# Optimization experiments

Hardware: AMD Instinct MI355X
Metric: run time of the kernel (lower is better)

## Reference

```python
import jax, jax.numpy as jnp
import numpy as np

B = 8192
I = 1024  # input_size
H = 1024  # hidden_size


def setup_inputs() -> dict:
    key = jax.random.key(0)
    ks = jax.random.split(key, 8)
    s_i = 1.0 / np.sqrt(I)
    s_h = 1.0 / np.sqrt(H)
    return {
        "x": jax.random.normal(ks[0], (B, I), dtype=jnp.float32),
        "h": jax.random.normal(ks[1], (B, H), dtype=jnp.float32),
        # nn.Linear weights have shape [out, in]; y = x @ W.T
        "W_wz": jax.random.uniform(ks[2], (H, I), jnp.float32, -s_i, s_i),
        "W_uz": jax.random.uniform(ks[3], (H, H), jnp.float32, -s_h, s_h),
        "W_wr": jax.random.uniform(ks[4], (H, I), jnp.float32, -s_i, s_i),
        "W_ur": jax.random.uniform(ks[5], (H, H), jnp.float32, -s_h, s_h),
        "W_u": jax.random.uniform(ks[6], (H, H), jnp.float32, -s_h, s_h),
        "W_w": jax.random.uniform(ks[7], (H, I), jnp.float32, -s_i, s_i),
    }


def reference(x, h, W_wz, W_uz, W_wr, W_ur, W_u, W_w):
    # Fuse the three x-projections and the two h-projections into grouped GEMMs.
    # [B, 3H] = x @ [I, 3H]
    xp = x @ jnp.concatenate([W_wz, W_wr, W_w], axis=0).T
    hp = h @ jnp.concatenate([W_uz, W_ur], axis=0).T  # [B, 2H]
    z = jax.nn.sigmoid(xp[:, :H] + hp[:, :H])
    r = jax.nn.sigmoid(xp[:, H:2 * H] + hp[:, H:])
    h_t = jnp.tanh((r * h) @ W_u.T + xp[:, 2 * H:])
    return z * h + (1.0 - z) * h_t
```

## Files before the change

kernel.cpp:

```cpp
#include <hip/hip_runtime.h>

typedef unsigned short u16;
typedef __attribute__((ext_vector_type(8))) short bf16x8;
typedef __attribute__((ext_vector_type(4))) float f32x4;

__device__ __forceinline__ u16 f2b(float f) {
  unsigned u = __float_as_uint(f);
  u += 0x7FFFu + ((u >> 16) & 1u);
  return (u16)(u >> 16);
}
__device__ __forceinline__ float sigm(float x) { return 1.0f / (1.0f + __expf(-x)); }
__device__ __forceinline__ float tanh_f(float x) { return 1.0f - 2.0f / (__expf(2.0f * x) + 1.0f); }

__device__ __forceinline__ void cp16(const u16* g, u16* l) {
  __builtin_amdgcn_global_load_lds(
      (const __attribute__((address_space(1))) unsigned int*)g,
      (__attribute__((address_space(3))) unsigned int*)l, 16, 0, 0);
}

__device__ __forceinline__ int swz(int b) {
  return b ^ (((b >> 7) & 3) << 5) ^ (((b >> 9) & 1) << 4);
}

__global__ __launch_bounds__(256) void pack_xh(const float* __restrict__ x,
                                               const float* __restrict__ h,
                                               u16* __restrict__ xhb) {
  int idx = blockIdx.x * 256 + threadIdx.x;
  int row = idx >> 9;
  int k = (idx & 511) << 2;
  const float* src = (k < 1024) ? (x + row * 1024 + k) : (h + row * 1024 + (k - 1024));
  float4 v = *reinterpret_cast<const float4*>(src);
  ushort4 o = make_ushort4(f2b(v.x), f2b(v.y), f2b(v.z), f2b(v.w));
  *reinterpret_cast<ushort4*>(xhb + ((size_t)idx << 2)) = o;
}

__global__ __launch_bounds__(256) void pack_w1(const float* __restrict__ Wwz,
                                               const float* __restrict__ Wuz,
                                               const float* __restrict__ Wwr,
                                               const float* __restrict__ Wur,
                                               const float* __restrict__ Ww,
                                               u16* __restrict__ W1b) {
  int idx = blockIdx.x * 256 + threadIdx.x;
  int n = idx >> 9;
  int k = (idx & 511) << 2;
  float4 v = make_float4(0.f, 0.f, 0.f, 0.f);
  if (n < 1024) {
    v = (k < 1024) ? *reinterpret_cast<const float4*>(Wwz + n * 1024 + k)
                   : *reinterpret_cast<const float4*>(Wuz + n * 1024 + (k - 1024));
  } else if (n < 2048) {
    int nn = n - 1024;
    v = (k < 1024) ? *reinterpret_cast<const float4*>(Wwr + nn * 1024 + k)
                   : *reinterpret_cast<const float4*>(Wur + nn * 1024 + (k - 1024));
  } else {
    int nn = n - 2048;
    if (k < 1024) v = *reinterpret_cast<const float4*>(Ww + nn * 1024 + k);
  }
  ushort4 o = make_ushort4(f2b(v.x), f2b(v.y), f2b(v.z), f2b(v.w));
  *reinterpret_cast<ushort4*>(W1b + ((size_t)idx << 2)) = o;
}

__global__ __launch_bounds__(256) void pack_wu(const float* __restrict__ Wu,
                                               u16* __restrict__ Wub) {
  int idx = blockIdx.x * 256 + threadIdx.x;
  float4 v = *reinterpret_cast<const float4*>(Wu + ((size_t)idx << 2));
  ushort4 o = make_ushort4(f2b(v.x), f2b(v.y), f2b(v.z), f2b(v.w));
  *reinterpret_cast<ushort4*>(Wub + ((size_t)idx << 2)) = o;
}

__device__ __forceinline__ void body(int t, int NT,
                                     const u16* __restrict__ Ag, const u16* __restrict__ Bg,
                                     int lda, int ldb,
                                     const u16* Ar, const u16* Br, u16* Aw, u16* Bw,
                                     int r0, int c2, int arl0, int arl1,
                                     int wr, int wc, int tid, f32x4 acc[4][4]) {
  const int ab = wr * 4096;
  const int bb = wc * 4096;
  bf16x8 af0[2][2], bfr[4][2];
#pragma unroll
  for (int mm = 0; mm < 2; ++mm) {
    af0[mm][0] = *reinterpret_cast<const bf16x8*>(Ar + ab + mm * 1024 + arl0);
    af0[mm][1] = *reinterpret_cast<const bf16x8*>(Ar + ab + mm * 1024 + arl1);
  }
#pragma unroll
  for (int nf = 0; nf < 4; ++nf) {
    bfr[nf][0] = *reinterpret_cast<const bf16x8*>(Br + bb + nf * 1024 + arl0);
    bfr[nf][1] = *reinterpret_cast<const bf16x8*>(Br + bb + nf * 1024 + arl1);
  }
  if (t + 1 < NT) {
    const u16* g0 = Ag + (size_t)r0 * lda + c2 + (size_t)(t + 1) * 64;
    u16* l0 = Aw + tid * 8;
    cp16(g0, l0); cp16(g0 + (size_t)64 * lda, l0 + 4096);
    const u16* g1 = Ag + (size_t)(128 + r0) * lda + c2 + (size_t)(t + 1) * 64;
    u16* l1 = Aw + 8192 + tid * 8;
    cp16(g1, l1); cp16(g1 + (size_t)64 * lda, l1 + 4096);
  }
  __builtin_amdgcn_s_barrier();
  __builtin_amdgcn_s_setprio(1);
#pragma unroll
  for (int mm = 0; mm < 2; ++mm)
#pragma unroll
    for (int nf = 0; nf < 4; ++nf)
#pragma unroll
      for (int ks = 0; ks < 2; ++ks)
        acc[mm][nf] = __builtin_amdgcn_mfma_f32_16x16x32_bf16(
            af0[mm][ks], bfr[nf][ks], acc[mm][nf], 0, 0, 0);
  __builtin_amdgcn_s_setprio(0);
  __builtin_amdgcn_s_barrier();
  bf16x8 af1[2][2];
#pragma unroll
  for (int mm = 0; mm < 2; ++mm) {
    af1[mm][0] = *reinterpret_cast<const bf16x8*>(Ar + ab + (2 + mm) * 1024 + arl0);
    af1[mm][1] = *reinterpret_cast<const bf16x8*>(Ar + ab + (2 + mm) * 1024 + arl1);
  }
  if (t + 2 < NT) {
    const u16* g = Bg + (size_t)r0 * ldb + c2 + (size_t)(t + 2) * 64;
    u16* l = Bw + tid * 8;
    cp16(g, l); cp16(g + (size_t)64 * ldb, l + 4096);
    asm volatile("s_waitcnt vmcnt(2)" ::: "memory");
  } else {
    asm volatile("s_waitcnt vmcnt(0)" ::: "memory");
  }
  __builtin_amdgcn_s_barrier();
  __builtin_amdgcn_s_setprio(1);
#pragma unroll
  for (int mm = 0; mm < 2; ++mm)
#pragma unroll
    for (int nf = 0; nf < 4; ++nf)
#pragma unroll
      for (int ks = 0; ks < 2; ++ks)
        acc[2 + mm][nf] = __builtin_amdgcn_mfma_f32_16x16x32_bf16(
            af1[mm][ks], bfr[nf][ks], acc[2 + mm][nf], 0, 0, 0);
  __builtin_amdgcn_s_setprio(0);
  __builtin_amdgcn_s_barrier();
}

__device__ __forceinline__ void core(const u16* __restrict__ Ag, const u16* __restrict__ Bg,
                                     int lda, int ldb, int NT,
                                     u16* As0, u16* As1, u16* Bs0, u16* Bs1,
                                     f32x4 acc[4][4]) {
  const int tid = threadIdx.x;
  const int lane = tid & 63;
  const int wid = tid >> 6;
  const int wr = wid >> 1;
  const int wc = wid & 1;

  const int plo = tid * 16;
  const int olo = swz(plo);
  const int r0 = olo >> 7;
  const int c2 = (olo & 127) >> 1;

  const int frow = lane & 15;
  const int fcb = (lane >> 4) * 16;
  const int mask = ((frow & 3) << 5) | (((frow >> 2) & 1) << 4);
  const int arl0 = (frow * 128 + ((fcb + 0) ^ mask)) >> 1;
  const int arl1 = (frow * 128 + ((fcb + 64) ^ mask)) >> 1;

  {
    const u16* g; u16* l;
    g = Ag + (size_t)r0 * lda + c2;          l = As0 + tid * 8;        cp16(g, l); cp16(g + (size_t)64 * lda, l + 4096);
    g = Ag + (size_t)(128 + r0) * lda + c2;  l = As0 + 8192 + tid * 8; cp16(g, l); cp16(g + (size_t)64 * lda, l + 4096);
    g = Bg + (size_t)r0 * ldb + c2;          l = Bs0 + tid * 8;        cp16(g, l); cp16(g + (size_t)64 * ldb, l + 4096);
    g = Bg + (size_t)r0 * ldb + c2 + 64;     l = Bs1 + tid * 8;        cp16(g, l); cp16(g + (size_t)64 * ldb, l + 4096);
  }
  asm volatile("s_waitcnt vmcnt(2)" ::: "memory");
  __builtin_amdgcn_s_barrier();

  for (int u = 0; u < NT; u += 2) {
    body(u,     NT, Ag, Bg, lda, ldb, As0, Bs0, As1, Bs0, r0, c2, arl0, arl1, wr, wc, tid, acc);
    body(u + 1, NT, Ag, Bg, lda, ldb, As1, Bs1, As0, Bs1, r0, c2, arl0, arl1, wr, wc, tid, acc);
  }
}

#define CORE_PRE()                                           \
  __shared__ u16 As0[16384];                                 \
  __shared__ u16 As1[16384];                                 \
  __shared__ u16 Bs0[8192];                                  \
  __shared__ u16 Bs1[8192];                                  \
  f32x4 acc[4][4];                                           \
  _Pragma("unroll") for (int m = 0; m < 4; ++m)              \
  _Pragma("unroll") for (int n = 0; n < 4; ++n)              \
      acc[m][n] = (f32x4){0.f, 0.f, 0.f, 0.f};

__global__ __launch_bounds__(512, 2) void gemm_zr(const u16* __restrict__ xhb,
                                                  const u16* __restrict__ W1b,
                                                  const float* __restrict__ h,
                                                  float* __restrict__ zout,
                                                  u16* __restrict__ rhb) {
  int b = blockIdx.x;
  int wg = (b & 7) * 64 + (b >> 3);
  int nb = wg >> 5, mb = wg & 31;
  const int m0 = mb * 256, n0 = nb * 128;
  CORE_PRE();
  core(xhb + (size_t)m0 * 2048, W1b + (size_t)n0 * 2048, 2048, 2048, 32,
       As0, As1, Bs0, Bs1, acc);

  const int lane = threadIdx.x & 63;
  const int wid = threadIdx.x >> 6;
  const int wr = wid >> 1, wc = wid & 1;
  const int rbase = m0 + wr * 64 + ((lane >> 4) << 2);
  const int cbase = n0 + wc * 64 + (lane & 15);
  const int isz = (n0 < 1024);
#pragma unroll
  for (int m = 0; m < 4; ++m) {
#pragma unroll
    for (int nf = 0; nf < 4; ++nf) {
      const int col = cbase + nf * 16;
#pragma unroll
      for (int j = 0; j < 4; ++j) {
        const int row = rbase + m * 16 + j;
        const float v = acc[m][nf][j];
        if (isz) {
          zout[(size_t)row * 1024 + col] = sigm(v);
        } else {
          const size_t idx = (size_t)row * 1024 + (col - 1024);
          rhb[idx] = f2b(sigm(v) * h[idx]);
        }
      }
    }
  }
}

__global__ __launch_bounds__(512, 2) void gemm_w(const u16* __restrict__ xhb,
                                                 const u16* __restrict__ W1b,
                                                 float* __restrict__ xwb) {
  int b = blockIdx.x;
  int wg = (b & 7) * 32 + (b >> 3);
  int nb = wg >> 5, mb = wg & 31;
  const int m0 = mb * 256, n0 = nb * 128;
  CORE_PRE();
  core(xhb + (size_t)m0 * 2048, W1b + (size_t)(2048 + n0) * 2048, 2048, 2048, 16,
       As0, As1, Bs0, Bs1, acc);

  const int lane = threadIdx.x & 63;
  const int wid = threadIdx.x >> 6;
  const int wr = wid >> 1, wc = wid & 1;
  const int rbase = m0 + wr * 64 + ((lane >> 4) << 2);
  const int cbase = n0 + wc * 64 + (lane & 15);
#pragma unroll
  for (int m = 0; m < 4; ++m)
#pragma unroll
    for (int nf = 0; nf < 4; ++nf)
#pragma unroll
      for (int j = 0; j < 4; ++j)
        xwb[(size_t)(rbase + m * 16 + j) * 1024 + cbase + nf * 16] = acc[m][nf][j];
}

__global__ __launch_bounds__(512, 2) void gemm2_k(const u16* __restrict__ rhb,
                                                  const u16* __restrict__ Wub,
                                                  const float* __restrict__ h,
                                                  const float* __restrict__ xwb,
                                                  float* __restrict__ out) {
  int b = blockIdx.x;
  int wg = (b & 7) * 32 + (b >> 3);
  int nb = wg >> 5, mb = wg & 31;
  const int m0 = mb * 256, n0 = nb * 128;
  CORE_PRE();
  core(rhb + (size_t)m0 * 1024, Wub + (size_t)n0 * 1024, 1024, 1024, 16,
       As0, As1, Bs0, Bs1, acc);

  const int lane = threadIdx.x & 63;
  const int wid = threadIdx.x >> 6;
  const int wr = wid >> 1, wc = wid & 1;
  const int rbase = m0 + wr * 64 + ((lane >> 4) << 2);
  const int cbase = n0 + wc * 64 + (lane & 15);
#pragma unroll
  for (int m = 0; m < 4; ++m) {
#pragma unroll
    for (int nf = 0; nf < 4; ++nf) {
      const int col = cbase + nf * 16;
#pragma unroll
      for (int j = 0; j < 4; ++j) {
        const int row = rbase + m * 16 + j;
        const size_t idx = (size_t)row * 1024 + col;
        const float z = out[idx];
        const float hv = h[idx];
        const float ht = tanh_f(acc[m][nf][j] + xwb[idx]);
        out[idx] = z * hv + (1.0f - z) * ht;
      }
    }
  }
}

extern "C" void kernel_launch(void* const* d_in, const int* in_sizes, int n_in,
                              void* d_out, int out_size, void* d_ws, size_t ws_size,
                              hipStream_t stream) {
  const float* x   = (const float*)d_in[0];
  const float* h   = (const float*)d_in[1];
  const float* Wwz = (const float*)d_in[2];
  const float* Wuz = (const float*)d_in[3];
  const float* Wwr = (const float*)d_in[4];
  const float* Wur = (const float*)d_in[5];
  const float* Wu  = (const float*)d_in[6];
  const float* Ww  = (const float*)d_in[7];
  float* out = (float*)d_out;

  char* ws = (char*)d_ws;
  u16*   xhb = (u16*)(ws);
  u16*   W1b = (u16*)(ws + 33554432);
  u16*   Wub = (u16*)(ws + 46137344);
  u16*   rhb = (u16*)(ws + 48234496);
  float* xwb = (float*)(ws + 65011712);

  pack_xh<<<16384, 256, 0, stream>>>(x, h, xhb);
  pack_w1<<<6144, 256, 0, stream>>>(Wwz, Wuz, Wwr, Wur, Ww, W1b);
  pack_wu<<<1024, 256, 0, stream>>>(Wu, Wub);
  gemm_zr<<<512, 512, 0, stream>>>(xhb, W1b, h, out, rhb);
  gemm_w<<<256, 512, 0, stream>>>(xhb, W1b, xwb);
  gemm2_k<<<256, 512, 0, stream>>>(rhb, Wub, h, xwb, out);
}
```

Baseline: 336.0 us.

## Triple-buffer GEMM LDS pipeline, remap block tiles, store x-projection in bf16

The GEMM main loop moves from double to triple buffering in LDS, so A and B tiles are prefetched two k-steps ahead, with a relaxed vmcnt wait placed after the MFMAs. The block-index to tile mapping is swapped so consecutive workgroups walk the N dimension instead of M, which changes L2 reuse. The intermediate x@W_w projection is stored as bf16 instead of fp32 to halve its write and read traffic. LDS use per block rises to about 144KB, which likely stops two 512-thread blocks from fitting on one CU, and the bf16 intermediate adds rounding error.

```diff
diff --git a/kernel.cpp b/kernel.cpp
--- a/kernel.cpp
+++ b/kernel.cpp
@@ -9,6 +9,7 @@
   u += 0x7FFFu + ((u >> 16) & 1u);
   return (u16)(u >> 16);
 }
+__device__ __forceinline__ float b2f(u16 v) { return __uint_as_float(((unsigned)v) << 16); }
 __device__ __forceinline__ float sigm(float x) { return 1.0f / (1.0f + __expf(-x)); }
 __device__ __forceinline__ float tanh_f(float x) { return 1.0f - 2.0f / (__expf(2.0f * x) + 1.0f); }
 
@@ -75,6 +76,7 @@
                                      int wr, int wc, int tid, f32x4 acc[4][4]) {
   const int ab = wr * 4096;
   const int bb = wc * 4096;
+  const bool pf = (t + 2 < NT);
   bf16x8 af0[2][2], bfr[4][2];
 #pragma unroll
   for (int mm = 0; mm < 2; ++mm) {
@@ -86,11 +88,11 @@
     bfr[nf][0] = *reinterpret_cast<const bf16x8*>(Br + bb + nf * 1024 + arl0);
     bfr[nf][1] = *reinterpret_cast<const bf16x8*>(Br + bb + nf * 1024 + arl1);
   }
-  if (t + 1 < NT) {
-    const u16* g0 = Ag + (size_t)r0 * lda + c2 + (size_t)(t + 1) * 64;
+  if (pf) {
+    const u16* g0 = Ag + (size_t)r0 * lda + c2 + (size_t)(t + 2) * 64;
     u16* l0 = Aw + tid * 8;
     cp16(g0, l0); cp16(g0 + (size_t)64 * lda, l0 + 4096);
-    const u16* g1 = Ag + (size_t)(128 + r0) * lda + c2 + (size_t)(t + 1) * 64;
+    const u16* g1 = Ag + (size_t)(128 + r0) * lda + c2 + (size_t)(t + 2) * 64;
     u16* l1 = Aw + 8192 + tid * 8;
     cp16(g1, l1); cp16(g1 + (size_t)64 * lda, l1 + 4096);
   }
@@ -112,13 +114,10 @@
     af1[mm][0] = *reinterpret_cast<const bf16x8*>(Ar + ab + (2 + mm) * 1024 + arl0);
     af1[mm][1] = *reinterpret_cast<const bf16x8*>(Ar + ab + (2 + mm) * 1024 + arl1);
   }
-  if (t + 2 < NT) {
+  if (pf) {
     const u16* g = Bg + (size_t)r0 * ldb + c2 + (size_t)(t + 2) * 64;
     u16* l = Bw + tid * 8;
     cp16(g, l); cp16(g + (size_t)64 * ldb, l + 4096);
-    asm volatile("s_waitcnt vmcnt(2)" ::: "memory");
-  } else {
-    asm volatile("s_waitcnt vmcnt(0)" ::: "memory");
   }
   __builtin_amdgcn_s_barrier();
   __builtin_amdgcn_s_setprio(1);
@@ -131,12 +130,15 @@
         acc[2 + mm][nf] = __builtin_amdgcn_mfma_f32_16x16x32_bf16(
             af1[mm][ks], bfr[nf][ks], acc[2 + mm][nf], 0, 0, 0);
   __builtin_amdgcn_s_setprio(0);
+  if (pf) asm volatile("s_waitcnt vmcnt(6)" ::: "memory");
+  else    asm volatile("s_waitcnt vmcnt(0)" ::: "memory");
   __builtin_amdgcn_s_barrier();
 }
 
 __device__ __forceinline__ void core(const u16* __restrict__ Ag, const u16* __restrict__ Bg,
                                      int lda, int ldb, int NT,
-                                     u16* As0, u16* As1, u16* Bs0, u16* Bs1,
+                                     u16* As0, u16* As1, u16* As2,
+                                     u16* Bs0, u16* Bs1, u16* Bs2,
                                      f32x4 acc[4][4]) {
   const int tid = threadIdx.x;
   const int lane = tid & 63;
@@ -155,27 +157,41 @@
   const int arl0 = (frow * 128 + ((fcb + 0) ^ mask)) >> 1;
   const int arl1 = (frow * 128 + ((fcb + 64) ^ mask)) >> 1;
 
-  {
-    const u16* g; u16* l;
-    g = Ag + (size_t)r0 * lda + c2;          l = As0 + tid * 8;        cp16(g, l); cp16(g + (size_t)64 * lda, l + 4096);
-    g = Ag + (size_t)(128 + r0) * lda + c2;  l = As0 + 8192 + tid * 8; cp16(g, l); cp16(g + (size_t)64 * lda, l + 4096);
-    g = Bg + (size_t)r0 * ldb + c2;          l = Bs0 + tid * 8;        cp16(g, l); cp16(g + (size_t)64 * ldb, l + 4096);
-    g = Bg + (size_t)r0 * ldb + c2 + 64;     l = Bs1 + tid * 8;        cp16(g, l); cp16(g + (size_t)64 * ldb, l + 4096);
-  }
-  asm volatile("s_waitcnt vmcnt(2)" ::: "memory");
-  __builtin_amdgcn_s_barrier();
-
-  for (int u = 0; u < NT; u += 2) {
-    body(u,     NT, Ag, Bg, lda, ldb, As0, Bs0, As1, Bs0, r0, c2, arl0, arl1, wr, wc, tid, acc);
-    body(u + 1, NT, Ag, Bg, lda, ldb, As1, Bs1, As0, Bs1, r0, c2, arl0, arl1, wr, wc, tid, acc);
+  auto stA = [&](u16* buf, int tg) {
+    const u16* g0 = Ag + (size_t)r0 * lda + c2 + (size_t)tg * 64;
+    u16* l0 = buf + tid * 8;
+    cp16(g0, l0); cp16(g0 + (size_t)64 * lda, l0 + 4096);
+    const u16* g1 = Ag + (size_t)(128 + r0) * lda + c2 + (size_t)tg * 64;
+    u16* l1 = buf + 8192 + tid * 8;
+    cp16(g1, l1); cp16(g1 + (size_t)64 * lda, l1 + 4096);
+  };
+  auto stB = [&](u16* buf, int tg) {
+    const u16* g = Bg + (size_t)r0 * ldb + c2 + (size_t)tg * 64;
+    u16* l = buf + tid * 8;
+    cp16(g, l); cp16(g + (size_t)64 * ldb, l + 4096);
+  };
+
+  stA(As0, 0); stB(Bs0, 0);
+  stA(As1, 1); stB(Bs1, 1);
+  asm volatile("s_waitcnt vmcnt(6)" ::: "memory");
+  __builtin_amdgcn_s_barrier();
+
+  for (int u = 0; u < NT; u += 3) {
+    body(u, NT, Ag, Bg, lda, ldb, As0, Bs0, As2, Bs2, r0, c2, arl0, arl1, wr, wc, tid, acc);
+    if (u + 1 < NT)
+      body(u + 1, NT, Ag, Bg, lda, ldb, As1, Bs1, As0, Bs0, r0, c2, arl0, arl1, wr, wc, tid, acc);
+    if (u + 2 < NT)
+      body(u + 2, NT, Ag, Bg, lda, ldb, As2, Bs2, As1, Bs1, r0, c2, arl0, arl1, wr, wc, tid, acc);
   }
 }
 
 #define CORE_PRE()                                           \
   __shared__ u16 As0[16384];                                 \
   __shared__ u16 As1[16384];                                 \
+  __shared__ u16 As2[16384];                                 \
   __shared__ u16 Bs0[8192];                                  \
   __shared__ u16 Bs1[8192];                                  \
+  __shared__ u16 Bs2[8192];                                  \
   f32x4 acc[4][4];                                           \
   _Pragma("unroll") for (int m = 0; m < 4; ++m)              \
   _Pragma("unroll") for (int n = 0; n < 4; ++n)              \
@@ -188,11 +204,11 @@
                                                   u16* __restrict__ rhb) {
   int b = blockIdx.x;
   int wg = (b & 7) * 64 + (b >> 3);
-  int nb = wg >> 5, mb = wg & 31;
+  int mb = wg >> 4, nb = wg & 15;
   const int m0 = mb * 256, n0 = nb * 128;
   CORE_PRE();
   core(xhb + (size_t)m0 * 2048, W1b + (size_t)n0 * 2048, 2048, 2048, 32,
-       As0, As1, Bs0, Bs1, acc);
+       As0, As1, As2, Bs0, Bs1, Bs2, acc);
 
   const int lane = threadIdx.x & 63;
   const int wid = threadIdx.x >> 6;
@@ -222,14 +238,14 @@
 
 __global__ __launch_bounds__(512, 2) void gemm_w(const u16* __restrict__ xhb,
                                                  const u16* __restrict__ W1b,
-                                                 float* __restrict__ xwb) {
+                                                 u16* __restrict__ xwb) {
   int b = blockIdx.x;
   int wg = (b & 7) * 32 + (b >> 3);
-  int nb = wg >> 5, mb = wg & 31;
+  int mb = wg >> 3, nb = wg & 7;
   const int m0 = mb * 256, n0 = nb * 128;
   CORE_PRE();
   core(xhb + (size_t)m0 * 2048, W1b + (size_t)(2048 + n0) * 2048, 2048, 2048, 16,
-       As0, As1, Bs0, Bs1, acc);
+       As0, As1, As2, Bs0, Bs1, Bs2, acc);
 
   const int lane = threadIdx.x & 63;
   const int wid = threadIdx.x >> 6;
@@ -242,21 +258,21 @@
     for (int nf = 0; nf < 4; ++nf)
 #pragma unroll
       for (int j = 0; j < 4; ++j)
-        xwb[(size_t)(rbase + m * 16 + j) * 1024 + cbase + nf * 16] = acc[m][nf][j];
+        xwb[(size_t)(rbase + m * 16 + j) * 1024 + cbase + nf * 16] = f2b(acc[m][nf][j]);
 }
 
 __global__ __launch_bounds__(512, 2) void gemm2_k(const u16* __restrict__ rhb,
                                                   const u16* __restrict__ Wub,
                                                   const float* __restrict__ h,
-                                                  const float* __restrict__ xwb,
+                                                  const u16* __restrict__ xwb,
                                                   float* __restrict__ out) {
   int b = blockIdx.x;
   int wg = (b & 7) * 32 + (b >> 3);
-  int nb = wg >> 5, mb = wg & 31;
+  int mb = wg >> 3, nb = wg & 7;
   const int m0 = mb * 256, n0 = nb * 128;
   CORE_PRE();
   core(rhb + (size_t)m0 * 1024, Wub + (size_t)n0 * 1024, 1024, 1024, 16,
-       As0, As1, Bs0, Bs1, acc);
+       As0, As1, As2, Bs0, Bs1, Bs2, acc);
 
   const int lane = threadIdx.x & 63;
   const int wid = threadIdx.x >> 6;
@@ -274,7 +290,7 @@
         const size_t idx = (size_t)row * 1024 + col;
         const float z = out[idx];
         const float hv = h[idx];
-        const float ht = tanh_f(acc[m][nf][j] + xwb[idx]);
+        const float ht = tanh_f(acc[m][nf][j] + b2f(xwb[idx]));
         out[idx] = z * hv + (1.0f - z) * ht;
       }
     }
@@ -299,7 +315,7 @@
   u16*   W1b = (u16*)(ws + 33554432);
   u16*   Wub = (u16*)(ws + 46137344);
   u16*   rhb = (u16*)(ws + 48234496);
-  float* xwb = (float*)(ws + 65011712);
+  u16*   xwb = (u16*)(ws + 65011712);
 
   pack_xh<<<16384, 256, 0, stream>>>(x, h, xhb);
   pack_w1<<<6144, 256, 0, stream>>>(Wwz, Wuz, Wwr, Wur, Ww, W1b);
```

Result: faster. 308.1 us (-8.3%).

## Fold x@Ww into second GEMM via concatenated K and drop zero-padded work

Applied to the files above, without the earlier changes.

The separate x@Ww GEMM and its fp32 intermediate are removed. The second GEMM now runs over a concatenated [r*h | x] operand against [Wu | Ww] with K=2048, so the candidate pre-activation is accumulated directly. This also drops the zero-padded half of the old W1 packing and merges the pack kernels with 8-wide conversions. It adds a second copy of x in bf16, changes the tile-order mapping, and relaxes the occupancy hint in launch bounds.

```diff
diff --git a/kernel.cpp b/kernel.cpp
--- a/kernel.cpp
+++ b/kernel.cpp
@@ -2,6 +2,7 @@
 
 typedef unsigned short u16;
 typedef __attribute__((ext_vector_type(8))) short bf16x8;
+typedef __attribute__((ext_vector_type(8))) unsigned short u16x8;
 typedef __attribute__((ext_vector_type(4))) float f32x4;
 
 __device__ __forceinline__ u16 f2b(float f) {
@@ -22,49 +23,59 @@
   return b ^ (((b >> 7) & 3) << 5) ^ (((b >> 9) & 1) << 4);
 }
 
+__device__ __forceinline__ u16x8 cvt8(float4 a, float4 b) {
+  u16x8 v;
+  v[0] = f2b(a.x); v[1] = f2b(a.y); v[2] = f2b(a.z); v[3] = f2b(a.w);
+  v[4] = f2b(b.x); v[5] = f2b(b.y); v[6] = f2b(b.z); v[7] = f2b(b.w);
+  return v;
+}
+
 __global__ __launch_bounds__(256) void pack_xh(const float* __restrict__ x,
                                                const float* __restrict__ h,
-                                               u16* __restrict__ xhb) {
+                                               u16* __restrict__ xhb,
+                                               u16* __restrict__ A2) {
   int idx = blockIdx.x * 256 + threadIdx.x;
-  int row = idx >> 9;
-  int k = (idx & 511) << 2;
-  const float* src = (k < 1024) ? (x + row * 1024 + k) : (h + row * 1024 + (k - 1024));
-  float4 v = *reinterpret_cast<const float4*>(src);
-  ushort4 o = make_ushort4(f2b(v.x), f2b(v.y), f2b(v.z), f2b(v.w));
-  *reinterpret_cast<ushort4*>(xhb + ((size_t)idx << 2)) = o;
-}
-
-__global__ __launch_bounds__(256) void pack_w1(const float* __restrict__ Wwz,
-                                               const float* __restrict__ Wuz,
-                                               const float* __restrict__ Wwr,
-                                               const float* __restrict__ Wur,
-                                               const float* __restrict__ Ww,
-                                               u16* __restrict__ W1b) {
+  int row = idx >> 8;
+  int k = (idx & 255) << 3;
+  const float* src = (k < 1024) ? (x + (size_t)row * 1024 + k)
+                                : (h + (size_t)row * 1024 + (k - 1024));
+  float4 a = *reinterpret_cast<const float4*>(src);
+  float4 b = *reinterpret_cast<const float4*>(src + 4);
+  u16x8 v = cvt8(a, b);
+  *reinterpret_cast<u16x8*>(xhb + ((size_t)row << 11) + k) = v;
+  if (k < 1024)
+    *reinterpret_cast<u16x8*>(A2 + ((size_t)row << 11) + 1024 + k) = v;
+}
+
+__global__ __launch_bounds__(256) void pack_W(const float* __restrict__ Wwz,
+                                              const float* __restrict__ Wuz,
+                                              const float* __restrict__ Wwr,
+                                              const float* __restrict__ Wur,
+                                              const float* __restrict__ Wu,
+                                              const float* __restrict__ Ww,
+                                              u16* __restrict__ W1b,
+                                              u16* __restrict__ W2b) {
   int idx = blockIdx.x * 256 + threadIdx.x;
-  int n = idx >> 9;
-  int k = (idx & 511) << 2;
-  float4 v = make_float4(0.f, 0.f, 0.f, 0.f);
-  if (n < 1024) {
-    v = (k < 1024) ? *reinterpret_cast<const float4*>(Wwz + n * 1024 + k)
-                   : *reinterpret_cast<const float4*>(Wuz + n * 1024 + (k - 1024));
-  } else if (n < 2048) {
-    int nn = n - 1024;
-    v = (k < 1024) ? *reinterpret_cast<const float4*>(Wwr + nn * 1024 + k)
-                   : *reinterpret_cast<const float4*>(Wur + nn * 1024 + (k - 1024));
+  const float* src;
+  u16* dst;
+  if (idx < 524288) {
+    int row = idx >> 8;
+    int k = (idx & 255) << 3;
+    const float* lo = (row < 1024) ? Wwz : Wwr;
+    const float* hi = (row < 1024) ? Wuz : Wur;
+    int n = row & 1023;
+    src = (k < 1024) ? (lo + (size_t)n * 1024 + k) : (hi + (size_t)n * 1024 + (k - 1024));
+    dst = W1b + ((size_t)row << 11) + k;
   } else {
-    int nn = n - 2048;
-    if (k < 1024) v = *reinterpret_cast<const float4*>(Ww + nn * 1024 + k);
-  }
-  ushort4 o = make_ushort4(f2b(v.x), f2b(v.y), f2b(v.z), f2b(v.w));
-  *reinterpret_cast<ushort4*>(W1b + ((size_t)idx << 2)) = o;
-}
-
-__global__ __launch_bounds__(256) void pack_wu(const float* __restrict__ Wu,
-                                               u16* __restrict__ Wub) {
-  int idx = blockIdx.x * 256 + threadIdx.x;
-  float4 v = *reinterpret_cast<const float4*>(Wu + ((size_t)idx << 2));
-  ushort4 o = make_ushort4(f2b(v.x), f2b(v.y), f2b(v.z), f2b(v.w));
-  *reinterpret_cast<ushort4*>(Wub + ((size_t)idx << 2)) = o;
+    int j = idx - 524288;
+    int row = j >> 8;
+    int k = (j & 255) << 3;
+    src = (k < 1024) ? (Wu + (size_t)row * 1024 + k) : (Ww + (size_t)row * 1024 + (k - 1024));
+    dst = W2b + ((size_t)row << 11) + k;
+  }
+  float4 a = *reinterpret_cast<const float4*>(src);
+  float4 b = *reinterpret_cast<const float4*>(src + 4);
+  *reinterpret_cast<u16x8*>(dst) = cvt8(a, b);
 }
 
 __device__ __forceinline__ void body(int t, int NT,
@@ -181,14 +192,14 @@
   _Pragma("unroll") for (int n = 0; n < 4; ++n)              \
       acc[m][n] = (f32x4){0.f, 0.f, 0.f, 0.f};
 
-__global__ __launch_bounds__(512, 2) void gemm_zr(const u16* __restrict__ xhb,
-                                                  const u16* __restrict__ W1b,
-                                                  const float* __restrict__ h,
-                                                  float* __restrict__ zout,
-                                                  u16* __restrict__ rhb) {
+__global__ __launch_bounds__(512) void gemm_zr(const u16* __restrict__ xhb,
+                                               const u16* __restrict__ W1b,
+                                               const float* __restrict__ h,
+                                               float* __restrict__ zout,
+                                               u16* __restrict__ A2) {
   int b = blockIdx.x;
   int wg = (b & 7) * 64 + (b >> 3);
-  int nb = wg >> 5, mb = wg & 31;
+  int mb = wg >> 4, nb = wg & 15;
   const int m0 = mb * 256, n0 = nb * 128;
   CORE_PRE();
   core(xhb + (size_t)m0 * 2048, W1b + (size_t)n0 * 2048, 2048, 2048, 32,
@@ -212,23 +223,25 @@
         if (isz) {
           zout[(size_t)row * 1024 + col] = sigm(v);
         } else {
-          const size_t idx = (size_t)row * 1024 + (col - 1024);
-          rhb[idx] = f2b(sigm(v) * h[idx]);
+          const int c = col - 1024;
+          const float rh = sigm(v) * h[(size_t)row * 1024 + c];
+          A2[((size_t)row << 11) + c] = f2b(rh);
         }
       }
     }
   }
 }
 
-__global__ __launch_bounds__(512, 2) void gemm_w(const u16* __restrict__ xhb,
-                                                 const u16* __restrict__ W1b,
-                                                 float* __restrict__ xwb) {
+__global__ __launch_bounds__(512) void gemm2_k(const u16* __restrict__ A2,
+                                               const u16* __restrict__ W2b,
+                                               const float* __restrict__ h,
+                                               float* __restrict__ out) {
   int b = blockIdx.x;
   int wg = (b & 7) * 32 + (b >> 3);
-  int nb = wg >> 5, mb = wg & 31;
+  int mb = wg >> 3, nb = wg & 7;
   const int m0 = mb * 256, n0 = nb * 128;
   CORE_PRE();
-  core(xhb + (size_t)m0 * 2048, W1b + (size_t)(2048 + n0) * 2048, 2048, 2048, 16,
+  core(A2 + (size_t)m0 * 2048, W2b + (size_t)n0 * 2048, 2048, 2048, 32,
        As0, As1, Bs0, Bs1, acc);
 
   const int lane = threadIdx.x & 63;
@@ -237,33 +250,6 @@
   const int rbase = m0 + wr * 64 + ((lane >> 4) << 2);
   const int cbase = n0 + wc * 64 + (lane & 15);
 #pragma unroll
-  for (int m = 0; m < 4; ++m)
-#pragma unroll
-    for (int nf = 0; nf < 4; ++nf)
-#pragma unroll
-      for (int j = 0; j < 4; ++j)
-        xwb[(size_t)(rbase + m * 16 + j) * 1024 + cbase + nf * 16] = acc[m][nf][j];
-}
-
-__global__ __launch_bounds__(512, 2) void gemm2_k(const u16* __restrict__ rhb,
-                                                  const u16* __restrict__ Wub,
-                                                  const float* __restrict__ h,
-                                                  const float* __restrict__ xwb,
-                                                  float* __restrict__ out) {
-  int b = blockIdx.x;
-  int wg = (b & 7) * 32 + (b >> 3);
-  int nb = wg >> 5, mb = wg & 31;
-  const int m0 = mb * 256, n0 = nb * 128;
-  CORE_PRE();
-  core(rhb + (size_t)m0 * 1024, Wub + (size_t)n0 * 1024, 1024, 1024, 16,
-       As0, As1, Bs0, Bs1, acc);
-
-  const int lane = threadIdx.x & 63;
-  const int wid = threadIdx.x >> 6;
-  const int wr = wid >> 1, wc = wid & 1;
-  const int rbase = m0 + wr * 64 + ((lane >> 4) << 2);
-  const int cbase = n0 + wc * 64 + (lane & 15);
-#pragma unroll
   for (int m = 0; m < 4; ++m) {
 #pragma unroll
     for (int nf = 0; nf < 4; ++nf) {
@@ -274,7 +260,7 @@
         const size_t idx = (size_t)row * 1024 + col;
         const float z = out[idx];
         const float hv = h[idx];
-        const float ht = tanh_f(acc[m][nf][j] + xwb[idx]);
+        const float ht = tanh_f(acc[m][nf][j]);
         out[idx] = z * hv + (1.0f - z) * ht;
       }
     }
@@ -295,16 +281,13 @@
   float* out = (float*)d_out;
 
   char* ws = (char*)d_ws;
-  u16*   xhb = (u16*)(ws);
-  u16*   W1b = (u16*)(ws + 33554432);
-  u16*   Wub = (u16*)(ws + 46137344);
-  u16*   rhb = (u16*)(ws + 48234496);
-  float* xwb = (float*)(ws + 65011712);
-
-  pack_xh<<<16384, 256, 0, stream>>>(x, h, xhb);
-  pack_w1<<<6144, 256, 0, stream>>>(Wwz, Wuz, Wwr, Wur, Ww, W1b);
-  pack_wu<<<1024, 256, 0, stream>>>(Wu, Wub);
-  gemm_zr<<<512, 512, 0, stream>>>(xhb, W1b, h, out, rhb);
-  gemm_w<<<256, 512, 0, stream>>>(xhb, W1b, xwb);
-  gemm2_k<<<256, 512, 0, stream>>>(rhb, Wub, h, xwb, out);
-}
+  u16* xhb = (u16*)(ws);
+  u16* A2  = (u16*)(ws + 33554432);
+  u16* W1b = (u16*)(ws + 67108864);
+  u16* W2b = (u16*)(ws + 75497472);
+
+  pack_xh<<<8192, 256, 0, stream>>>(x, h, xhb, A2);
+  pack_W<<<3072, 256, 0, stream>>>(Wwz, Wuz, Wwr, Wur, Wu, Ww, W1b, W2b);
+  gemm_zr<<<512, 512, 0, stream>>>(xhb, W1b, h, out, A2);
+  gemm2_k<<<256, 512, 0, stream>>>(A2, W2b, h, out);
+}
```

Result: faster. 313.0 us (-6.8%).
